# Kernel tuning notes

Hardware: AMD Instinct MI355X
Metric: run time of the kernel (lower is better)

The kernel has to match this reference:

```python
import jax, jax.numpy as jnp
import numpy as np

N = 50000      # nodes
E = 400000     # edges (before self-loops)
F_IN = 128     # input_embedding_dim
HID = 256      # hidden_dim
HEADS = 4      # gat_heads
C1 = HID // HEADS  # per-head channels layer 0
OUT = 128      # output_node_dim
G = 64         # graphs in batch
NEG_SLOPE = 0.2


def setup_inputs() -> dict:
    key = jax.random.key(0)
    ks = jax.random.split(key, 12)
    s = lambda fan: 1.0 / np.sqrt(fan)
    embedded_x = jax.random.normal(ks[0], (N, F_IN), jnp.float32)
    edge_index = jax.random.randint(ks[1], (2, E), 0, N, dtype=jnp.int32)
    batch_idx = jnp.sort(jax.random.randint(ks[2], (N,), 0, G, dtype=jnp.int32))
    # layer 0: GATConv(F_IN -> C1, heads=HEADS, concat=True)
    W1 = jax.random.normal(ks[3], (F_IN, HEADS * C1), jnp.float32) * s(F_IN)
    att_src1 = jax.random.normal(ks[4], (HEADS, C1), jnp.float32) * s(C1)
    att_dst1 = jax.random.normal(ks[5], (HEADS, C1), jnp.float32) * s(C1)
    b1 = jnp.zeros((HEADS * C1,), jnp.float32)
    # layer 1 (last): GATConv(HID -> OUT, heads=1, concat=False)
    W2 = jax.random.normal(ks[6], (HID, OUT), jnp.float32) * s(HID)
    att_src2 = jax.random.normal(ks[7], (1, OUT), jnp.float32) * s(OUT)
    att_dst2 = jax.random.normal(ks[8], (1, OUT), jnp.float32) * s(OUT)
    b2 = jnp.zeros((OUT,), jnp.float32)
    return {"embedded_x": embedded_x, "edge_index": edge_index, "batch_idx": batch_idx,
            "W1": W1, "att_src1": att_src1, "att_dst1": att_dst1, "b1": b1,
            "W2": W2, "att_src2": att_src2, "att_dst2": att_dst2, "b2": b2}


def gat_conv(x, src, dst, W, att_src, att_dst, bias, heads, out_ch, concat):
    n = x.shape[0]
    xw = (x @ W).reshape(n, heads, out_ch)              # [N,H,C]
    a_s = (xw * att_src[None]).sum(-1)                  # [N,H]
    a_d = (xw * att_dst[None]).sum(-1)                  # [N,H]
    e = jax.nn.leaky_relu(a_s[src] + a_d[dst], NEG_SLOPE)  # [E',H]
    # segment softmax over incoming edges of each dst node (self-loops guarantee non-empty)
    m = jax.ops.segment_max(e, dst, num_segments=n)
    ee = jnp.exp(e - m[dst])
    denom = jax.ops.segment_sum(ee, dst, num_segments=n)
    alpha = ee / denom[dst]                             # [E',H]
    msg = xw[src] * alpha[:, :, None]                   # [E',H,C]
    out = jax.ops.segment_sum(msg, dst, num_segments=n) # [N,H,C]
    out = out.reshape(n, heads * out_ch) if concat else out.mean(axis=1)
    return out + bias


def reference(embedded_x, edge_index, batch_idx, W1, att_src1, att_dst1, b1, W2, att_src2, att_dst2, b2):
    loops = jnp.arange(N, dtype=edge_index.dtype)
    src = jnp.concatenate([edge_index[0], loops])
    dst = jnp.concatenate([edge_index[1], loops])
    h = gat_conv(embedded_x, src, dst, W1, att_src1, att_dst1, b1, HEADS, C1, True)
    h = jax.nn.elu(h)  # dropout is identity in eval
    h = gat_conv(h, src, dst, W2, att_src2, att_dst2, b2, 1, OUT, False)
    h = jax.nn.elu(h)
    # final_node_transform is Identity (current_dim == output_node_dim)
    counts = jax.ops.segment_sum(jnp.ones((N,), h.dtype), batch_idx, num_segments=G)
    graph_embedding = jax.ops.segment_sum(h, batch_idx, num_segments=G) / jnp.maximum(counts, 1.0)[:, None]
    return (graph_embedding, h)
```

## Files before the change

### kernel.cpp

```cpp
#include <hip/hip_runtime.h>

#define NN   50000
#define NE   400000
#define NET  450000
#define NG   64
#define NEG  0.2f
#define BCAP 32

#define GEMM1_BLOCKS 782
#define FILL_BLOCKS  318
#define FUSE_BLOCKS  (GEMM1_BLOCKS + FILL_BLOCKS)

using bf16x8 = __attribute__((ext_vector_type(8))) short;
using f32x4  = __attribute__((ext_vector_type(4))) float;

__device__ inline float b2f(unsigned short u){
  union{unsigned int i; float f;} v; v.i = ((unsigned int)u) << 16; return v.f;
}
__device__ inline unsigned short f2b(float f){
  union{float f; unsigned int i;} v; v.f = f;
  unsigned int r = (v.i + 0x7fffu + ((v.i >> 16) & 1u)) >> 16;
  return (unsigned short)r;
}
__device__ inline float sane(float o){
  return (o > -1e30f && o < 1e30f) ? o : 0.f;
}
__device__ inline float lrelu_clamp(float e){
  e = fmaxf(e, NEG * e);
  return fminf(e, 60.f);
}

__device__ inline void pack_one(const float* W, unsigned short* Bp, int t, int K, int N){
  int nk = K / 32;
  int lane = t & 63; int rest = t >> 6;
  int kit = rest % nk; int nt = rest / nk;
  int quad = lane >> 4, n = lane & 15;
  unsigned short* dst = Bp + (size_t)t * 8;
#pragma unroll
  for (int j = 0; j < 8; j++)
    dst[j] = f2b(W[(size_t)(kit*32 + quad*8 + j) * N + nt*16 + n]);
}
__global__ void init_kernel(int* __restrict__ bcnt, float* __restrict__ pools, int* __restrict__ cnt,
                            const float* __restrict__ W1, const float* __restrict__ W2,
                            unsigned short* __restrict__ Bp1, unsigned short* __restrict__ Bp2){
  int i = blockIdx.x * 256 + threadIdx.x;
  if (i < NN) bcnt[i] = 0;
  if (i < NG * 128) pools[i] = 0.f;
  if (i < NG) cnt[i] = 0;
  if (i < 4096)                 pack_one(W1, Bp1, i, 128, 256);
  else if (i < 8192)            pack_one(W2, Bp2, i - 4096, 256, 128);
}

__device__ void gemm1_body(int vb, const float* __restrict__ X, const unsigned short* __restrict__ Bp,
                           const float* __restrict__ av, const float* __restrict__ dv,
                           unsigned short* __restrict__ C,
                           float* __restrict__ a_s, float* __restrict__ a_d){
  constexpr int NK = 4, NT = 16;
  int lane = threadIdx.x & 63, wave = threadIdx.x >> 6;
  int mbase = (vb * 4 + wave) * 16;
  if (mbase >= NN) return;
  int quad = lane >> 4, nn = lane & 15;
  int arow = mbase + nn; if (arow >= NN) arow = NN - 1;
  const float* Xr = X + (size_t)arow * 128 + quad * 8;
  bf16x8 afrag[NK];
#pragma unroll
  for (int kit = 0; kit < NK; kit++){
    bf16x8 a;
#pragma unroll
    for (int j = 0; j < 8; j++) a[j] = (short)f2b(Xr[kit * 32 + j]);
    afrag[kit] = a;
  }
  float sd0=0,sd1=0,sd2=0,sd3=0, dd0=0,dd1=0,dd2=0,dd3=0;
#pragma unroll
  for (int nt = 0; nt < NT; nt++){
    f32x4 acc = {0.f, 0.f, 0.f, 0.f};
#pragma unroll
    for (int kit = 0; kit < NK; kit++){
      bf16x8 bfrag = *(const bf16x8*)(Bp + ((size_t)(nt*NK + kit) * 64 + lane) * 8);
      acc = __builtin_amdgcn_mfma_f32_16x16x32_bf16(afrag[kit], bfrag, acc, 0, 0, 0);
    }
    int col = nt * 16 + nn;
    float avc = av[col], dvc = dv[col];
    sd0 += acc[0]*avc; dd0 += acc[0]*dvc;
    sd1 += acc[1]*avc; dd1 += acc[1]*dvc;
    sd2 += acc[2]*avc; dd2 += acc[2]*dvc;
    sd3 += acc[3]*avc; dd3 += acc[3]*dvc;
#pragma unroll
    for (int r = 0; r < 4; r++){
      int row = mbase + quad * 4 + r;
      if (row < NN) C[(size_t)row * 256 + col] = f2b(acc[r]);
    }
    if ((nt & 3) == 3){
      int hh = nt >> 2;
#pragma unroll
      for (int off = 1; off < 16; off <<= 1){
        sd0 += __shfl_xor(sd0, off); sd1 += __shfl_xor(sd1, off);
        sd2 += __shfl_xor(sd2, off); sd3 += __shfl_xor(sd3, off);
        dd0 += __shfl_xor(dd0, off); dd1 += __shfl_xor(dd1, off);
        dd2 += __shfl_xor(dd2, off); dd3 += __shfl_xor(dd3, off);
      }
      if (nn == 0){
        int row = mbase + quad * 4;
        if (row + 0 < NN){ a_s[(row+0)*4+hh] = sd0; a_d[(row+0)*4+hh] = dd0; }
        if (row + 1 < NN){ a_s[(row+1)*4+hh] = sd1; a_d[(row+1)*4+hh] = dd1; }
        if (row + 2 < NN){ a_s[(row+2)*4+hh] = sd2; a_d[(row+2)*4+hh] = dd2; }
        if (row + 3 < NN){ a_s[(row+3)*4+hh] = sd3; a_d[(row+3)*4+hh] = dd3; }
      }
      sd0=sd1=sd2=sd3=dd0=dd1=dd2=dd3=0.f;
    }
  }
}

__global__ void gemm1_fill(const float* __restrict__ X, const unsigned short* __restrict__ Bp,
                           const float* __restrict__ av, const float* __restrict__ dv,
                           unsigned short* __restrict__ C,
                           float* __restrict__ a_s, float* __restrict__ a_d,
                           const int* __restrict__ ei, int* __restrict__ bcnt,
                           int* __restrict__ csr){
  int b = blockIdx.x;
  if (b < GEMM1_BLOCKS){
    gemm1_body(b, X, Bp, av, dv, C, a_s, a_d);
  } else {
    const int STR = FILL_BLOCKS * 256;
    for (int t = (b - GEMM1_BLOCKS) * 256 + threadIdx.x; t < NET; t += STR){
      int s = (t < NE) ? ei[t]      : (t - NE);
      int d = (t < NE) ? ei[NE + t] : (t - NE);
      if (d < 0) d = 0; if (d >= NN) d = NN - 1;
      int pos = atomicAdd(&bcnt[d], 1);
      if (pos < BCAP) csr[d * BCAP + pos] = s;
    }
  }
}

__global__ void agg1(const unsigned short* __restrict__ xw, const float* __restrict__ a_s,
                     const float* __restrict__ a_d, const int* __restrict__ bcnt,
                     const int* __restrict__ csr, const float* __restrict__ bias,
                     unsigned short* __restrict__ h1){
  int lane = threadIdx.x & 63;
  int node = (blockIdx.x * blockDim.x + threadIdx.x) >> 6;
  if (node >= NN) return;
  int h = lane >> 4;
  int beg = node * BCAP;
  int cv = bcnt[node]; if (cv > BCAP) cv = BCAP; if (cv < 0) cv = 0;
  int end = beg + cv;
  float adv = a_d[node * 4 + h];
  float l0=0,l1=0,l2=0,l3=0;
  float c00=0,c01=0,c02=0,c03=0;
  float c10=0,c11=0,c12=0,c13=0;
  float c20=0,c21=0,c22=0,c23=0;
  float c30=0,c31=0,c32=0,c33=0;
  int e = beg;
  for (; e + 4 <= end; e += 4){
    int s0 = csr[e], s1 = csr[e+1], s2 = csr[e+2], s3 = csr[e+3];
    float p0 = __expf(lrelu_clamp(a_s[s0*4+h] + adv));
    float p1 = __expf(lrelu_clamp(a_s[s1*4+h] + adv));
    float p2 = __expf(lrelu_clamp(a_s[s2*4+h] + adv));
    float p3 = __expf(lrelu_clamp(a_s[s3*4+h] + adv));
    ushort4 x0 = *(const ushort4*)(xw + (size_t)s0 * 256 + lane * 4);
    ushort4 x1 = *(const ushort4*)(xw + (size_t)s1 * 256 + lane * 4);
    ushort4 x2 = *(const ushort4*)(xw + (size_t)s2 * 256 + lane * 4);
    ushort4 x3 = *(const ushort4*)(xw + (size_t)s3 * 256 + lane * 4);
    l0 += p0; c00 += p0*b2f(x0.x); c01 += p0*b2f(x0.y); c02 += p0*b2f(x0.z); c03 += p0*b2f(x0.w);
    l1 += p1; c10 += p1*b2f(x1.x); c11 += p1*b2f(x1.y); c12 += p1*b2f(x1.z); c13 += p1*b2f(x1.w);
    l2 += p2; c20 += p2*b2f(x2.x); c21 += p2*b2f(x2.y); c22 += p2*b2f(x2.z); c23 += p2*b2f(x2.w);
    l3 += p3; c30 += p3*b2f(x3.x); c31 += p3*b2f(x3.y); c32 += p3*b2f(x3.z); c33 += p3*b2f(x3.w);
  }
  for (; e < end; e++){
    int s0 = csr[e];
    float p0 = __expf(lrelu_clamp(a_s[s0*4+h] + adv));
    ushort4 x0 = *(const ushort4*)(xw + (size_t)s0 * 256 + lane * 4);
    l0 += p0; c00 += p0*b2f(x0.x); c01 += p0*b2f(x0.y); c02 += p0*b2f(x0.z); c03 += p0*b2f(x0.w);
  }
  float l = (l0 + l1) + (l2 + l3);
  float C0 = (c00 + c10) + (c20 + c30);
  float C1 = (c01 + c11) + (c21 + c31);
  float C2 = (c02 + c12) + (c22 + c32);
  float C3 = (c03 + c13) + (c23 + c33);
  if (!(l > 0.f)) l = 1.f;
  float inv = 1.f / l;
  float4 b4 = *(const float4*)(bias + lane * 4);
  float v; ushort4 o;
  v = C0 * inv + b4.x; v = v > 0.f ? v : expm1f(v); o.x = f2b(sane(v));
  v = C1 * inv + b4.y; v = v > 0.f ? v : expm1f(v); o.y = f2b(sane(v));
  v = C2 * inv + b4.z; v = v > 0.f ? v : expm1f(v); o.z = f2b(sane(v));
  v = C3 * inv + b4.w; v = v > 0.f ? v : expm1f(v); o.w = f2b(sane(v));
  *(ushort4*)(h1 + (size_t)node * 256 + lane * 4) = o;
}

__global__ void gemm2_fused(const unsigned short* __restrict__ A, const unsigned short* __restrict__ Bp,
                            const float* __restrict__ av, const float* __restrict__ dv,
                            unsigned short* __restrict__ C,
                            float* __restrict__ a_s, float* __restrict__ a_d){
  constexpr int NK = 8, NT = 8;
  int lane = threadIdx.x & 63, wave = threadIdx.x >> 6;
  int mbase = (blockIdx.x * 4 + wave) * 16;
  if (mbase >= NN) return;
  int quad = lane >> 4, nn = lane & 15;
  int arow = mbase + nn; if (arow >= NN) arow = NN - 1;
  const unsigned short* Ar = A + (size_t)arow * 256 + quad * 8;
  bf16x8 afrag[NK];
#pragma unroll
  for (int kit = 0; kit < NK; kit++)
    afrag[kit] = *(const bf16x8*)(Ar + kit * 32);
  float sd0=0,sd1=0,sd2=0,sd3=0, dd0=0,dd1=0,dd2=0,dd3=0;
#pragma unroll
  for (int nt = 0; nt < NT; nt++){
    f32x4 acc = {0.f, 0.f, 0.f, 0.f};
#pragma unroll
    for (int kit = 0; kit < NK; kit++){
      bf16x8 bfrag = *(const bf16x8*)(Bp + ((size_t)(nt*NK + kit) * 64 + lane) * 8);
      acc = __builtin_amdgcn_mfma_f32_16x16x32_bf16(afrag[kit], bfrag, acc, 0, 0, 0);
    }
    int col = nt * 16 + nn;
    float avc = av[col], dvc = dv[col];
    sd0 += acc[0]*avc; dd0 += acc[0]*dvc;
    sd1 += acc[1]*avc; dd1 += acc[1]*dvc;
    sd2 += acc[2]*avc; dd2 += acc[2]*dvc;
    sd3 += acc[3]*avc; dd3 += acc[3]*dvc;
#pragma unroll
    for (int r = 0; r < 4; r++){
      int row = mbase + quad * 4 + r;
      if (row < NN) C[(size_t)row * 128 + col] = f2b(acc[r]);
    }
  }
#pragma unroll
  for (int off = 1; off < 16; off <<= 1){
    sd0 += __shfl_xor(sd0, off); sd1 += __shfl_xor(sd1, off);
    sd2 += __shfl_xor(sd2, off); sd3 += __shfl_xor(sd3, off);
    dd0 += __shfl_xor(dd0, off); dd1 += __shfl_xor(dd1, off);
    dd2 += __shfl_xor(dd2, off); dd3 += __shfl_xor(dd3, off);
  }
  if (nn == 0){
    int row = mbase + quad * 4;
    if (row + 0 < NN){ a_s[row+0] = sd0; a_d[row+0] = dd0; }
    if (row + 1 < NN){ a_s[row+1] = sd1; a_d[row+1] = dd1; }
    if (row + 2 < NN){ a_s[row+2] = sd2; a_d[row+2] = dd2; }
    if (row + 3 < NN){ a_s[row+3] = sd3; a_d[row+3] = dd3; }
  }
}

__global__ void agg2(const unsigned short* __restrict__ xw, const float* __restrict__ a_s,
                     const float* __restrict__ a_d, const int* __restrict__ bcnt,
                     const int* __restrict__ csr, const float* __restrict__ bias,
                     float* __restrict__ hout){
  int lane = threadIdx.x & 63;
  int node = (blockIdx.x * blockDim.x + threadIdx.x) >> 6;
  if (node >= NN) return;
  int beg = node * BCAP;
  int cv = bcnt[node]; if (cv > BCAP) cv = BCAP; if (cv < 0) cv = 0;
  int end = beg + cv;
  float adv = a_d[node];
  float l0=0,l1=0,l2=0,l3=0;
  float c00=0,c01=0, c10=0,c11=0, c20=0,c21=0, c30=0,c31=0;
  int e = beg;
  for (; e + 4 <= end; e += 4){
    int s0 = csr[e], s1 = csr[e+1], s2 = csr[e+2], s3 = csr[e+3];
    float p0 = __expf(lrelu_clamp(a_s[s0] + adv));
    float p1 = __expf(lrelu_clamp(a_s[s1] + adv));
    float p2 = __expf(lrelu_clamp(a_s[s2] + adv));
    float p3 = __expf(lrelu_clamp(a_s[s3] + adv));
    ushort2 x0 = *(const ushort2*)(xw + (size_t)s0 * 128 + lane * 2);
    ushort2 x1 = *(const ushort2*)(xw + (size_t)s1 * 128 + lane * 2);
    ushort2 x2 = *(const ushort2*)(xw + (size_t)s2 * 128 + lane * 2);
    ushort2 x3 = *(const ushort2*)(xw + (size_t)s3 * 128 + lane * 2);
    l0 += p0; c00 += p0*b2f(x0.x); c01 += p0*b2f(x0.y);
    l1 += p1; c10 += p1*b2f(x1.x); c11 += p1*b2f(x1.y);
    l2 += p2; c20 += p2*b2f(x2.x); c21 += p2*b2f(x2.y);
    l3 += p3; c30 += p3*b2f(x3.x); c31 += p3*b2f(x3.y);
  }
  for (; e < end; e++){
    int s0 = csr[e];
    float p0 = __expf(lrelu_clamp(a_s[s0] + adv));
    ushort2 x0 = *(const ushort2*)(xw + (size_t)s0 * 128 + lane * 2);
    l0 += p0; c00 += p0*b2f(x0.x); c01 += p0*b2f(x0.y);
  }
  float l = (l0 + l1) + (l2 + l3);
  float C0 = (c00 + c10) + (c20 + c30);
  float C1 = (c01 + c11) + (c21 + c31);
  if (!(l > 0.f)) l = 1.f;
  float inv = 1.f / l;
  float v0 = C0 * inv + bias[lane*2];   v0 = v0 > 0.f ? v0 : expm1f(v0);
  float v1 = C1 * inv + bias[lane*2+1]; v1 = v1 > 0.f ? v1 : expm1f(v1);
  float2 o; o.x = sane(v0); o.y = sane(v1);
  *(float2*)(hout + (size_t)node * 128 + lane * 2) = o;
}

__global__ void pool_kernel(const float* __restrict__ h, const int* __restrict__ batch,
                            float* __restrict__ pools, int* __restrict__ cnt){
  int c = threadIdx.x;
  int n0 = blockIdx.x * 16;
  if (n0 >= NN) return;
  int nend = n0 + 16; if (nend > NN) nend = NN;
  int cur = batch[n0];
  cur = (cur < 0) ? 0 : (cur >= NG ? NG - 1 : cur);
  float sum = 0.f; int count = 0;
  for (int n = n0; n < nend; n++){
    int g = batch[n];
    g = (g < 0) ? 0 : (g >= NG ? NG - 1 : g);
    if (g != cur){
      atomicAdd(&pools[cur * 128 + c], sum);
      if (c == 0) atomicAdd(&cnt[cur], count);
      sum = 0.f; count = 0; cur = g;
    }
    sum += h[(size_t)n * 128 + c];
    count++;
  }
  atomicAdd(&pools[cur * 128 + c], sum);
  if (c == 0) atomicAdd(&cnt[cur], count);
}

__global__ void final_kernel(const float* __restrict__ pools, const int* __restrict__ cnt,
                             float* __restrict__ out){
  int g = blockIdx.x, c = threadIdx.x;
  float d = fmaxf((float)cnt[g], 1.0f);
  out[g * 128 + c] = sane(pools[g * 128 + c] / d);
}

extern "C" void kernel_launch(void* const* d_in, const int* in_sizes, int n_in,
                              void* d_out, int out_size, void* d_ws, size_t ws_size,
                              hipStream_t stream){
  const float* x    = (const float*)d_in[0];
  const int*   ei   = (const int*)d_in[1];
  const int*   bat  = (const int*)d_in[2];
  const float* W1   = (const float*)d_in[3];
  const float* av1  = (const float*)d_in[4];
  const float* dv1  = (const float*)d_in[5];
  const float* b1   = (const float*)d_in[6];
  const float* W2   = (const float*)d_in[7];
  const float* av2  = (const float*)d_in[8];
  const float* dv2  = (const float*)d_in[9];
  const float* b2   = (const float*)d_in[10];

  char* w = (char*)d_ws;
  size_t o = 0;
  auto carve = [&](size_t bytes) -> char* {
    char* p = w + o; o += (bytes + 255) & ~(size_t)255; return p;
  };
  unsigned short* Bp1   = (unsigned short*)carve((size_t)4096 * 8 * 2);
  unsigned short* Bp2   = (unsigned short*)carve((size_t)4096 * 8 * 2);
  float*          a_s1v = (float*)carve((size_t)NN * 4 * 4);
  float*          a_d1v = (float*)carve((size_t)NN * 4 * 4);
  float*          a_s2v = (float*)carve((size_t)NN * 4);
  float*          a_d2v = (float*)carve((size_t)NN * 4);
  int*            bcnt  = (int*)carve((size_t)NN * 4);
  int*            csr   = (int*)carve((size_t)NN * BCAP * 4);
  float*          pools = (float*)carve((size_t)NG * 128 * 4);
  int*            cnt   = (int*)carve((size_t)NG * 4);
  unsigned short* xw1   = (unsigned short*)carve((size_t)NN * 256 * 2);
  unsigned short* h1b   = (unsigned short*)carve((size_t)NN * 256 * 2);
  unsigned short* xw2   = xw1;

  float* out_ge = (float*)d_out;
  float* out_h  = (float*)d_out + NG * 128;

  init_kernel<<<196, 256, 0, stream>>>(bcnt, pools, cnt, W1, W2, Bp1, Bp2);

  gemm1_fill<<<FUSE_BLOCKS, 256, 0, stream>>>(x, Bp1, av1, dv1, xw1, a_s1v, a_d1v,
                                              ei, bcnt, csr);

  agg1<<<12500, 256, 0, stream>>>(xw1, a_s1v, a_d1v, bcnt, csr, b1, h1b);

  gemm2_fused<<<782, 256, 0, stream>>>(h1b, Bp2, av2, dv2, xw2, a_s2v, a_d2v);
  agg2<<<12500, 256, 0, stream>>>(xw2, a_s2v, a_d2v, bcnt, csr, b2, out_h);

  pool_kernel<<<3125, 128, 0, stream>>>(out_h, bat, pools, cnt);
  final_kernel<<<NG, 128, 0, stream>>>(pools, cnt, out_ge);
}
```

Before: 246.6 us.

## Stage packed weights in LDS and run persistent GEMM blocks

Both GEMM kernels now copy the packed bf16 weight matrix (64 KB) into shared memory once per block. Each block then loops over several row tiles, so B fragments are read from LDS instead of L2 or global memory on every tile. The grid is cut to 256 GEMM blocks plus 256 fill blocks. This adds a per-block copy and barrier, and the 64 KB of LDS per block limits occupancy to about two blocks per CU.

New measurement: 260.2 us. 5.5% more time.

```diff
diff --git a/kernel.cpp b/kernel.cpp
--- a/kernel.cpp
+++ b/kernel.cpp
@@ -7,9 +7,10 @@
 #define NEG  0.2f
 #define BCAP 32
 
-#define GEMM1_BLOCKS 782
-#define FILL_BLOCKS  318
-#define FUSE_BLOCKS  (GEMM1_BLOCKS + FILL_BLOCKS)
+#define G1TILES 782
+#define G1B     256
+#define FILLB   256
+#define FUSEB   (G1B + FILLB)
 
 using bf16x8 = __attribute__((ext_vector_type(8))) short;
 using f32x4  = __attribute__((ext_vector_type(4))) float;
@@ -51,10 +52,10 @@
   else if (i < 8192)            pack_one(W2, Bp2, i - 4096, 256, 128);
 }
 
-__device__ void gemm1_body(int vb, const float* __restrict__ X, const unsigned short* __restrict__ Bp,
-                           const float* __restrict__ av, const float* __restrict__ dv,
-                           unsigned short* __restrict__ C,
-                           float* __restrict__ a_s, float* __restrict__ a_d){
+__device__ void gemm1_body_lds(int vb, const float* __restrict__ X, const unsigned short* Bs,
+                               const float* __restrict__ av, const float* __restrict__ dv,
+                               unsigned short* __restrict__ C,
+                               float* __restrict__ a_s, float* __restrict__ a_d){
   constexpr int NK = 4, NT = 16;
   int lane = threadIdx.x & 63, wave = threadIdx.x >> 6;
   int mbase = (vb * 4 + wave) * 16;
@@ -76,7 +77,7 @@
     f32x4 acc = {0.f, 0.f, 0.f, 0.f};
 #pragma unroll
     for (int kit = 0; kit < NK; kit++){
-      bf16x8 bfrag = *(const bf16x8*)(Bp + ((size_t)(nt*NK + kit) * 64 + lane) * 8);
+      bf16x8 bfrag = *(const bf16x8*)(Bs + ((size_t)(nt*NK + kit) * 64 + lane) * 8);
       acc = __builtin_amdgcn_mfma_f32_16x16x32_bf16(afrag[kit], bfrag, acc, 0, 0, 0);
     }
     int col = nt * 16 + nn;
@@ -111,18 +112,25 @@
   }
 }
 
-__global__ void gemm1_fill(const float* __restrict__ X, const unsigned short* __restrict__ Bp,
-                           const float* __restrict__ av, const float* __restrict__ dv,
-                           unsigned short* __restrict__ C,
-                           float* __restrict__ a_s, float* __restrict__ a_d,
-                           const int* __restrict__ ei, int* __restrict__ bcnt,
-                           int* __restrict__ csr){
+__global__ __launch_bounds__(256, 2)
+void gemm1_fill(const float* __restrict__ X, const unsigned short* __restrict__ Bp,
+                const float* __restrict__ av, const float* __restrict__ dv,
+                unsigned short* __restrict__ C,
+                float* __restrict__ a_s, float* __restrict__ a_d,
+                const int* __restrict__ ei, int* __restrict__ bcnt,
+                int* __restrict__ csr){
+  __shared__ unsigned short Bs[32768];
   int b = blockIdx.x;
-  if (b < GEMM1_BLOCKS){
-    gemm1_body(b, X, Bp, av, dv, C, a_s, a_d);
+  if (b < G1B){
+    const uint4* src = (const uint4*)Bp;
+    uint4* dst = (uint4*)Bs;
+    for (int i = threadIdx.x; i < 4096; i += 256) dst[i] = src[i];
+    __syncthreads();
+    for (int vb = b; vb < G1TILES; vb += G1B)
+      gemm1_body_lds(vb, X, Bs, av, dv, C, a_s, a_d);
   } else {
-    const int STR = FILL_BLOCKS * 256;
-    for (int t = (b - GEMM1_BLOCKS) * 256 + threadIdx.x; t < NET; t += STR){
+    const int STR = FILLB * 256;
+    for (int t = (b - G1B) * 256 + threadIdx.x; t < NET; t += STR){
       int s = (t < NE) ? ei[t]      : (t - NE);
       int d = (t < NE) ? ei[NE + t] : (t - NE);
       if (d < 0) d = 0; if (d >= NN) d = NN - 1;
@@ -187,13 +195,13 @@
   *(ushort4*)(h1 + (size_t)node * 256 + lane * 4) = o;
 }
 
-__global__ void gemm2_fused(const unsigned short* __restrict__ A, const unsigned short* __restrict__ Bp,
-                            const float* __restrict__ av, const float* __restrict__ dv,
-                            unsigned short* __restrict__ C,
-                            float* __restrict__ a_s, float* __restrict__ a_d){
+__device__ void gemm2_body_lds(int vb, const unsigned short* __restrict__ A, const unsigned short* Bs,
+                               const float* __restrict__ av, const float* __restrict__ dv,
+                               unsigned short* __restrict__ C,
+                               float* __restrict__ a_s, float* __restrict__ a_d){
   constexpr int NK = 8, NT = 8;
   int lane = threadIdx.x & 63, wave = threadIdx.x >> 6;
-  int mbase = (blockIdx.x * 4 + wave) * 16;
+  int mbase = (vb * 4 + wave) * 16;
   if (mbase >= NN) return;
   int quad = lane >> 4, nn = lane & 15;
   int arow = mbase + nn; if (arow >= NN) arow = NN - 1;
@@ -208,7 +216,7 @@
     f32x4 acc = {0.f, 0.f, 0.f, 0.f};
 #pragma unroll
     for (int kit = 0; kit < NK; kit++){
-      bf16x8 bfrag = *(const bf16x8*)(Bp + ((size_t)(nt*NK + kit) * 64 + lane) * 8);
+      bf16x8 bfrag = *(const bf16x8*)(Bs + ((size_t)(nt*NK + kit) * 64 + lane) * 8);
       acc = __builtin_amdgcn_mfma_f32_16x16x32_bf16(afrag[kit], bfrag, acc, 0, 0, 0);
     }
     int col = nt * 16 + nn;
@@ -237,6 +245,20 @@
     if (row + 2 < NN){ a_s[row+2] = sd2; a_d[row+2] = dd2; }
     if (row + 3 < NN){ a_s[row+3] = sd3; a_d[row+3] = dd3; }
   }
+}
+
+__global__ __launch_bounds__(256, 2)
+void gemm2_fused(const unsigned short* __restrict__ A, const unsigned short* __restrict__ Bp,
+                 const float* __restrict__ av, const float* __restrict__ dv,
+                 unsigned short* __restrict__ C,
+                 float* __restrict__ a_s, float* __restrict__ a_d){
+  __shared__ unsigned short Bs[32768];
+  const uint4* src = (const uint4*)Bp;
+  uint4* dst = (uint4*)Bs;
+  for (int i = threadIdx.x; i < 4096; i += 256) dst[i] = src[i];
+  __syncthreads();
+  for (int vb = blockIdx.x; vb < G1TILES; vb += G1B)
+    gemm2_body_lds(vb, A, Bs, av, dv, C, a_s, a_d);
 }
 
 __global__ void agg2(const unsigned short* __restrict__ xw, const float* __restrict__ a_s,
@@ -355,12 +377,12 @@
 
   init_kernel<<<196, 256, 0, stream>>>(bcnt, pools, cnt, W1, W2, Bp1, Bp2);
 
-  gemm1_fill<<<FUSE_BLOCKS, 256, 0, stream>>>(x, Bp1, av1, dv1, xw1, a_s1v, a_d1v,
-                                              ei, bcnt, csr);
+  gemm1_fill<<<FUSEB, 256, 0, stream>>>(x, Bp1, av1, dv1, xw1, a_s1v, a_d1v,
+                                        ei, bcnt, csr);
 
   agg1<<<12500, 256, 0, stream>>>(xw1, a_s1v, a_d1v, bcnt, csr, b1, h1b);
 
-  gemm2_fused<<<782, 256, 0, stream>>>(h1b, Bp2, av2, dv2, xw2, a_s2v, a_d2v);
+  gemm2_fused<<<G1B, 256, 0, stream>>>(h1b, Bp2, av2, dv2, xw2, a_s2v, a_d2v);
   agg2<<<12500, 256, 0, stream>>>(xw2, a_s2v, a_d2v, bcnt, csr, b2, out_h);
 
   pool_kernel<<<3125, 128, 0, stream>>>(out_h, bat, pools, cnt);
```
